# Performance work log

Hardware: AMD Instinct MI355X
Metric: run time of the kernel (lower is better)

Reference implementation:

```python
import jax, jax.numpy as jnp
import numpy as np

N_NODES = 50000
N_EDGES = 800000
D_IN = 128
HC = 128
D_OUT = 128
BN_EPS = 1e-5
RRELU_SLOPE = (1.0 / 8.0 + 1.0 / 3.0) / 2.0  # RReLU eval mode: (lower+upper)/2 = 11/48


def setup_inputs() -> dict:
    key = jax.random.key(0)
    ks = jax.random.split(key, 10)
    s_in = 1.0 / np.sqrt(D_IN)
    s_hc = 1.0 / np.sqrt(HC)
    return {
        "x": jax.random.normal(ks[0], (N_NODES, D_IN), jnp.float32),
        "edge_index": jax.random.randint(ks[1], (2, N_EDGES), 0, N_NODES),
        "edge_attr": jax.random.uniform(ks[2], (N_EDGES,), jnp.float32),
        # conv1: GraphConv(D_IN -> HC): lin_rel (with bias) + lin_root (no bias)
        "W1_rel": jax.random.normal(ks[3], (HC, D_IN), jnp.float32) * s_in,
        "b1": jnp.zeros((HC,), jnp.float32),
        "W1_root": jax.random.normal(ks[4], (HC, D_IN), jnp.float32) * s_in,
        # bn1 affine params
        "gamma": jnp.ones((HC,), jnp.float32),
        "beta": jnp.zeros((HC,), jnp.float32),
        # conv2: GraphConv(HC -> D_OUT)
        "W2_rel": jax.random.normal(ks[5], (D_OUT, HC), jnp.float32) * s_hc,
        "b2": jnp.zeros((D_OUT,), jnp.float32),
        "W2_root": jax.random.normal(ks[6], (D_OUT, HC), jnp.float32) * s_hc,
    }


def graph_conv(x, src, tgt, edge_w, W_rel, b_rel, W_root):
    # message: edge_weight * x[src]; aggregate: scatter-add into target nodes
    msg = x[src] * edge_w[:, None]                                   # [E, F]
    agg = jax.ops.segment_sum(msg, tgt, num_segments=x.shape[0])     # [N, F]
    return agg @ W_rel.T + b_rel + x @ W_root.T                      # [N, F_out]


def reference(x, edge_index, edge_attr, W1_rel, b1, W1_root, gamma, beta, W2_rel, b2, W2_root):
    src, tgt = edge_index[0], edge_index[1]
    h = graph_conv(x, src, tgt, edge_attr, W1_rel, b1, W1_root)      # [N, HC]
    # BatchNorm1d (training mode: biased batch stats over node dim)
    mean = h.mean(axis=0)
    var = h.var(axis=0)
    h = (h - mean) * jax.lax.rsqrt(var + BN_EPS) * gamma + beta
    # RReLU (deterministic eval slope)
    h = jnp.where(h >= 0, h, h * RRELU_SLOPE)
    return graph_conv(h, src, tgt, edge_attr, W2_rel, b2, W2_root)   # [N, D_OUT]
```

## Files before the change

### kernel.cpp

```cpp
#include <hip/hip_runtime.h>

#define N_NODES 50000
#define N_EDGES 800000
#define F 128
#define BN_EPS 1e-5f
#define SLOPE 0.22916666666666666f

#define NBKT 196
#define BKT_CAP 8192
#define P1_CHUNK 4096
#define P1_EPB 16
#define P1_BLKS 196
#define CASTX_BLKS 6250
#define CASTW_BLKS 64
#define BKT_FINAL_CAP 9984
#define REC_CAP 1160192
#define N_RT 3125
#define GEMM_GRID 512

typedef __attribute__((ext_vector_type(8))) short bf16x8;
typedef __attribute__((ext_vector_type(4))) float f32x4;
typedef unsigned long long u64;

__device__ __forceinline__ float bf2f(ushort u) {
    union { uint i; float f; } v; v.i = (uint)u << 16; return v.f;
}
__device__ __forceinline__ ushort f2bf(float f) {
    union { float f; uint i; } v; v.f = f;
    uint r = v.i + 0x7fffu + ((v.i >> 16) & 1u);
    return (ushort)(r >> 16);
}

__global__ __launch_bounds__(256) void s1p_k(const int* __restrict__ src,
        const int* __restrict__ tgt, const float* __restrict__ ew,
        int* __restrict__ bcur, u64* __restrict__ stg,
        const float* __restrict__ x, ushort* __restrict__ xb,
        const float* __restrict__ W1r, const float* __restrict__ W1t,
        const float* __restrict__ W2r, const float* __restrict__ W2t,
        ushort* __restrict__ wb) {
    const int b = blockIdx.x;
    if (b >= P1_BLKS) {
        if (b < P1_BLKS + CASTX_BLKS) {
            int i = (b - P1_BLKS) * 256 + threadIdx.x;
            float4 v = reinterpret_cast<const float4*>(x)[i];
            ushort4 o;
            o.x = f2bf(v.x); o.y = f2bf(v.y); o.z = f2bf(v.z); o.w = f2bf(v.w);
            reinterpret_cast<ushort4*>(xb)[i] = o;
        } else {
            int i = (b - P1_BLKS - CASTX_BLKS) * 256 + threadIdx.x;
            int m = i >> 12;
            int j = i & 4095;
            const float* sp = (m == 0) ? W1r : (m == 1) ? W1t : (m == 2) ? W2r : W2t;
            float4 v = reinterpret_cast<const float4*>(sp)[j];
            ushort4 o;
            o.x = f2bf(v.x); o.y = f2bf(v.y); o.z = f2bf(v.z); o.w = f2bf(v.w);
            reinterpret_cast<ushort4*>(wb)[i] = o;
        }
        return;
    }
    __shared__ uint cnt[256];
    __shared__ uint base[256];
    __shared__ uint lcur[256];
    __shared__ uint gbase[256];
    __shared__ u64 lrec[P1_CHUNK];

    const int e0 = b * P1_CHUNK;
    const int nE = min(P1_CHUNK, N_EDGES - e0);
    cnt[threadIdx.x] = 0;
    __syncthreads();

    u64 myrec[P1_EPB];
    bool myok[P1_EPB];
#pragma unroll
    for (int k = 0; k < P1_EPB; ++k) {
        int idx = threadIdx.x + (k << 8);
        bool ok = idx < nE;
        myok[k] = ok;
        if (ok) {
            int e = e0 + idx;
            uint t = (uint)tgt[e];
            uint lo = (uint)(ushort)src[e] | ((uint)f2bf(ew[e]) << 16);
            myrec[k] = (u64)lo | ((u64)t << 32);
            atomicAdd(&cnt[t >> 8], 1u);
        }
    }
    __syncthreads();
    uint v = cnt[threadIdx.x];
    base[threadIdx.x] = v;
    __syncthreads();
    for (int o = 1; o < 256; o <<= 1) {
        uint t = (threadIdx.x >= (unsigned)o) ? base[threadIdx.x - o] : 0;
        __syncthreads();
        base[threadIdx.x] += t;
        __syncthreads();
    }
    uint excl = base[threadIdx.x] - v;
    base[threadIdx.x] = excl;
    lcur[threadIdx.x] = excl;
    if (threadIdx.x < NBKT && v > 0)
        gbase[threadIdx.x] = (uint)threadIdx.x * BKT_CAP +
                             (uint)atomicAdd(&bcur[threadIdx.x], (int)v);
    __syncthreads();
#pragma unroll
    for (int k = 0; k < P1_EPB; ++k) {
        if (myok[k]) {
            uint bb = (uint)(myrec[k] >> 40);
            uint slot = atomicAdd(&lcur[bb], 1u);
            lrec[slot] = myrec[k];
        }
    }
    __syncthreads();
    for (int s = threadIdx.x; s < nE; s += 256) {
        u64 r = lrec[s];
        uint bb = (uint)(r >> 40);
        stg[gbase[bb] + ((uint)s - base[bb])] = r;
    }
}

__global__ __launch_bounds__(256) void sort2_k(const int* __restrict__ bcur,
        const u64* __restrict__ stg, uint* __restrict__ recs, int2* __restrict__ rng) {
    __shared__ int lcnt[256];
    __shared__ int lcur[256];
    __shared__ int sc[256];
    __shared__ int fbase_s;
    __shared__ uint lrec[BKT_FINAL_CAP];
    const int b = blockIdx.x;
    const int tid = threadIdx.x;

    int cnt_t = (tid < NBKT) ? bcur[tid] : 0;
    int stride_t = (tid < NBKT) ? (((cnt_t + 7) & ~7) + 1792) : 0;
    sc[tid] = stride_t;
    lcnt[tid] = 0;
    __syncthreads();
    for (int o = 1; o < 256; o <<= 1) {
        int t = (tid >= o) ? sc[tid - o] : 0;
        __syncthreads();
        sc[tid] += t;
        __syncthreads();
    }
    if (tid == b) fbase_s = sc[tid] - stride_t;
    __syncthreads();
    const int fbase = fbase_s;
    const int cnt = bcur[b];
    const u64* sb = stg + (size_t)b * BKT_CAP;

    for (int i = tid; i < cnt; i += 256)
        atomicAdd(&lcnt[(int)(sb[i] >> 32) & 255], 1);
    __syncthreads();
    const int node = b * 256 + tid;
    int myc = lcnt[tid];
    int myp = (myc + 7) & ~7;
    if (node >= N_NODES) myp = 0;
    sc[tid] = myp;
    __syncthreads();
    for (int o = 1; o < 256; o <<= 1) {
        int t = (tid >= o) ? sc[tid - o] : 0;
        __syncthreads();
        sc[tid] += t;
        __syncthreads();
    }
    const int myoff = sc[tid] - myp;
    const int ptot = sc[255];
    lcur[tid] = myoff;
    if (node < N_NODES) rng[node] = make_int2(fbase + myoff, fbase + myoff + myp);
    for (int i = tid; i < ptot; i += 256) lrec[i] = 0;
    __syncthreads();
    for (int i = tid; i < cnt; i += 256) {
        u64 r = sb[i];
        int n = (int)(r >> 32) & 255;
        int p = atomicAdd(&lcur[n], 1);
        lrec[p] = (uint)r;
    }
    __syncthreads();
    for (int i = tid; i < ptot; i += 256) recs[fbase + i] = lrec[i];
}

__global__ __launch_bounds__(256) void gather_k(const ushort* __restrict__ featb,
        const int2* __restrict__ rng, const uint* __restrict__ recs,
        ushort* __restrict__ aggb) {
    int node = blockIdx.x * 4 + (threadIdx.x >> 6);
    int lane2 = (threadIdx.x & 63) * 2;
    int2 r = rng[node];
    float a0 = 0.f, a1 = 0.f;
    for (int p = r.x; p < r.y; p += 8) {
        uint4 ra = *reinterpret_cast<const uint4*>(recs + p);
        uint4 rb = *reinterpret_cast<const uint4*>(recs + p + 4);
        uint u0 = *reinterpret_cast<const uint*>(featb + (size_t)(ra.x & 0xffffu) * F + lane2);
        uint u1 = *reinterpret_cast<const uint*>(featb + (size_t)(ra.y & 0xffffu) * F + lane2);
        uint u2 = *reinterpret_cast<const uint*>(featb + (size_t)(ra.z & 0xffffu) * F + lane2);
        uint u3 = *reinterpret_cast<const uint*>(featb + (size_t)(ra.w & 0xffffu) * F + lane2);
        uint u4 = *reinterpret_cast<const uint*>(featb + (size_t)(rb.x & 0xffffu) * F + lane2);
        uint u5 = *reinterpret_cast<const uint*>(featb + (size_t)(rb.y & 0xffffu) * F + lane2);
        uint u6 = *reinterpret_cast<const uint*>(featb + (size_t)(rb.z & 0xffffu) * F + lane2);
        uint u7 = *reinterpret_cast<const uint*>(featb + (size_t)(rb.w & 0xffffu) * F + lane2);
        float w0 = bf2f((ushort)(ra.x >> 16)), w1 = bf2f((ushort)(ra.y >> 16));
        float w2 = bf2f((ushort)(ra.z >> 16)), w3 = bf2f((ushort)(ra.w >> 16));
        float w4 = bf2f((ushort)(rb.x >> 16)), w5 = bf2f((ushort)(rb.y >> 16));
        float w6 = bf2f((ushort)(rb.z >> 16)), w7 = bf2f((ushort)(rb.w >> 16));
        a0 += w0 * bf2f((ushort)u0) + w1 * bf2f((ushort)u1)
            + w2 * bf2f((ushort)u2) + w3 * bf2f((ushort)u3)
            + w4 * bf2f((ushort)u4) + w5 * bf2f((ushort)u5)
            + w6 * bf2f((ushort)u6) + w7 * bf2f((ushort)u7);
        a1 += w0 * bf2f((ushort)(u0 >> 16)) + w1 * bf2f((ushort)(u1 >> 16))
            + w2 * bf2f((ushort)(u2 >> 16)) + w3 * bf2f((ushort)(u3 >> 16))
            + w4 * bf2f((ushort)(u4 >> 16)) + w5 * bf2f((ushort)(u5 >> 16))
            + w6 * bf2f((ushort)(u6 >> 16)) + w7 * bf2f((ushort)(u7 >> 16));
    }
    *reinterpret_cast<uint*>(aggb + (size_t)node * F + lane2) =
        (uint)f2bf(a0) | ((uint)f2bf(a1) << 16);
}

__global__ __launch_bounds__(256) void gemm_mfma(const ushort* __restrict__ R,
        const ushort* __restrict__ T, const ushort* __restrict__ Wr,
        const ushort* __restrict__ Wt, const float* __restrict__ bias,
        float* __restrict__ out, ushort* __restrict__ outh,
        float* __restrict__ S, float* __restrict__ S2, int fuse_bn) {
    const int lane = threadIdx.x & 63;
    const int wave = threadIdx.x >> 6;
    const int quad = lane >> 4;
    const int l16 = lane & 15;
    const int cb = wave * 32;

    bf16x8 bR[2][4], bT[2][4];
#pragma unroll
    for (int t = 0; t < 2; ++t)
#pragma unroll
        for (int s = 0; s < 4; ++s) {
            int col = cb + t * 16 + l16;
            int k0 = s * 32 + quad * 8;
            bR[t][s] = *reinterpret_cast<const bf16x8*>(Wr + col * F + k0);
            bT[t][s] = *reinterpret_cast<const bf16x8*>(Wt + col * F + k0);
        }
    const float bias0 = bias[cb + l16];
    const float bias1 = bias[cb + 16 + l16];

    float s0 = 0.f, q0 = 0.f, s1 = 0.f, q1 = 0.f;

    for (int rt = blockIdx.x; rt < N_RT; rt += GEMM_GRID) {
        const int row0 = rt * 16;
        const ushort* rA = R + (row0 + l16) * F + quad * 8;
        const ushort* tA = T + (row0 + l16) * F + quad * 8;
        bf16x8 aR0 = *reinterpret_cast<const bf16x8*>(rA);
        bf16x8 aR1 = *reinterpret_cast<const bf16x8*>(rA + 32);
        bf16x8 aR2 = *reinterpret_cast<const bf16x8*>(rA + 64);
        bf16x8 aR3 = *reinterpret_cast<const bf16x8*>(rA + 96);
        bf16x8 aT0 = *reinterpret_cast<const bf16x8*>(tA);
        bf16x8 aT1 = *reinterpret_cast<const bf16x8*>(tA + 32);
        bf16x8 aT2 = *reinterpret_cast<const bf16x8*>(tA + 64);
        bf16x8 aT3 = *reinterpret_cast<const bf16x8*>(tA + 96);

        f32x4 acc0 = {0.f, 0.f, 0.f, 0.f};
        f32x4 acc1 = {0.f, 0.f, 0.f, 0.f};
        acc0 = __builtin_amdgcn_mfma_f32_16x16x32_bf16(aR0, bR[0][0], acc0, 0, 0, 0);
        acc1 = __builtin_amdgcn_mfma_f32_16x16x32_bf16(aR0, bR[1][0], acc1, 0, 0, 0);
        acc0 = __builtin_amdgcn_mfma_f32_16x16x32_bf16(aR1, bR[0][1], acc0, 0, 0, 0);
        acc1 = __builtin_amdgcn_mfma_f32_16x16x32_bf16(aR1, bR[1][1], acc1, 0, 0, 0);
        acc0 = __builtin_amdgcn_mfma_f32_16x16x32_bf16(aR2, bR[0][2], acc0, 0, 0, 0);
        acc1 = __builtin_amdgcn_mfma_f32_16x16x32_bf16(aR2, bR[1][2], acc1, 0, 0, 0);
        acc0 = __builtin_amdgcn_mfma_f32_16x16x32_bf16(aR3, bR[0][3], acc0, 0, 0, 0);
        acc1 = __builtin_amdgcn_mfma_f32_16x16x32_bf16(aR3, bR[1][3], acc1, 0, 0, 0);
        acc0 = __builtin_amdgcn_mfma_f32_16x16x32_bf16(aT0, bT[0][0], acc0, 0, 0, 0);
        acc1 = __builtin_amdgcn_mfma_f32_16x16x32_bf16(aT0, bT[1][0], acc1, 0, 0, 0);
        acc0 = __builtin_amdgcn_mfma_f32_16x16x32_bf16(aT1, bT[0][1], acc0, 0, 0, 0);
        acc1 = __builtin_amdgcn_mfma_f32_16x16x32_bf16(aT1, bT[1][1], acc1, 0, 0, 0);
        acc0 = __builtin_amdgcn_mfma_f32_16x16x32_bf16(aT2, bT[0][2], acc0, 0, 0, 0);
        acc1 = __builtin_amdgcn_mfma_f32_16x16x32_bf16(aT2, bT[1][2], acc1, 0, 0, 0);
        acc0 = __builtin_amdgcn_mfma_f32_16x16x32_bf16(aT3, bT[0][3], acc0, 0, 0, 0);
        acc1 = __builtin_amdgcn_mfma_f32_16x16x32_bf16(aT3, bT[1][3], acc1, 0, 0, 0);

        const int r0 = row0 + quad * 4;
        if (fuse_bn) {
#pragma unroll
            for (int g = 0; g < 4; ++g) {
                float v0 = acc0[g] + bias0;
                float v1 = acc1[g] + bias1;
                outh[(r0 + g) * F + cb + l16] = f2bf(v0);
                outh[(r0 + g) * F + cb + 16 + l16] = f2bf(v1);
                s0 += v0; q0 += v0 * v0;
                s1 += v1; q1 += v1 * v1;
            }
        } else {
#pragma unroll
            for (int g = 0; g < 4; ++g) {
                out[(r0 + g) * F + cb + l16] = acc0[g] + bias0;
                out[(r0 + g) * F + cb + 16 + l16] = acc1[g] + bias1;
            }
        }
    }

    if (fuse_bn) {
        s0 += __shfl_down(s0, 32); s0 += __shfl_down(s0, 16);
        q0 += __shfl_down(q0, 32); q0 += __shfl_down(q0, 16);
        s1 += __shfl_down(s1, 32); s1 += __shfl_down(s1, 16);
        q1 += __shfl_down(q1, 32); q1 += __shfl_down(q1, 16);
        if (lane < 16) {
            unsafeAtomicAdd(&S[cb + lane], s0);
            unsafeAtomicAdd(&S2[cb + lane], q0);
            unsafeAtomicAdd(&S[cb + 16 + lane], s1);
            unsafeAtomicAdd(&S2[cb + 16 + lane], q1);
        }
    }
}

__global__ __launch_bounds__(256) void norm_act_k(const ushort* __restrict__ hraw,
        const float* __restrict__ S, const float* __restrict__ S2,
        const float* __restrict__ gamma, const float* __restrict__ beta,
        ushort* __restrict__ hb) {
    __shared__ float sc_s[128], sh_s[128];
    if (threadIdx.x < 128) {
        int j = threadIdx.x;
        float mean = S[j] * (1.f / N_NODES);
        float var = S2[j] * (1.f / N_NODES) - mean * mean;
        float inv = rsqrtf(var + BN_EPS);
        float sc = gamma[j] * inv;
        sc_s[j] = sc;
        sh_s[j] = beta[j] - mean * sc;
    }
    __syncthreads();
    int i = blockIdx.x * 256 + threadIdx.x;
    int cbase = (i & 31) * 4;
    uint2 u = reinterpret_cast<const uint2*>(hraw)[i];
    float4 v = make_float4(bf2f((ushort)u.x), bf2f((ushort)(u.x >> 16)),
                           bf2f((ushort)u.y), bf2f((ushort)(u.y >> 16)));
    float4 sc = *reinterpret_cast<const float4*>(&sc_s[cbase]);
    float4 sh = *reinterpret_cast<const float4*>(&sh_s[cbase]);
    v.x = v.x * sc.x + sh.x;
    v.y = v.y * sc.y + sh.y;
    v.z = v.z * sc.z + sh.z;
    v.w = v.w * sc.w + sh.w;
    v.x = v.x >= 0.f ? v.x : v.x * SLOPE;
    v.y = v.y >= 0.f ? v.y : v.y * SLOPE;
    v.z = v.z >= 0.f ? v.z : v.z * SLOPE;
    v.w = v.w >= 0.f ? v.w : v.w * SLOPE;
    uint2 o;
    o.x = (uint)f2bf(v.x) | ((uint)f2bf(v.y) << 16);
    o.y = (uint)f2bf(v.z) | ((uint)f2bf(v.w) << 16);
    reinterpret_cast<uint2*>(hb)[i] = o;
}

extern "C" void kernel_launch(void* const* d_in, const int* in_sizes, int n_in,
                              void* d_out, int out_size, void* d_ws, size_t ws_size,
                              hipStream_t stream) {
    const float* x     = (const float*)d_in[0];
    const int*   ei    = (const int*)d_in[1];
    const float* ea    = (const float*)d_in[2];
    const float* W1r   = (const float*)d_in[3];
    const float* b1    = (const float*)d_in[4];
    const float* W1t   = (const float*)d_in[5];
    const float* gamma = (const float*)d_in[6];
    const float* beta  = (const float*)d_in[7];
    const float* W2r   = (const float*)d_in[8];
    const float* b2    = (const float*)d_in[9];
    const float* W2t   = (const float*)d_in[10];
    float* out = (float*)d_out;

    char* ws = (char*)d_ws;
    size_t off = 0;
    u64*    stg   = (u64*)(ws + off);    off += (size_t)NBKT * BKT_CAP * 8;
    ushort* featb = (ushort*)(ws + off); off += (size_t)N_NODES * F * 2;
    uint*   recs  = (uint*)(ws + off);   off += (size_t)REC_CAP * 4;
    int*    bcur  = (int*)(ws + off);    off += 256 * 4;
    float*  S     = (float*)(ws + off);  off += 128 * 4;
    float*  S2    = (float*)(ws + off);  off += 128 * 4;
    int2*   rng   = (int2*)(ws + off);   off += (size_t)N_NODES * 8;
    ushort* wb    = (ushort*)(ws + off); off += 4 * 16384 * 2;
    ushort* aggb  = (ushort*)stg;
    ushort* hraw  = (ushort*)d_out;

    const int* srcp = ei;
    const int* tgtp = ei + N_EDGES;

    hipMemsetAsync(bcur, 0, 256 * 4 + 256 * 4, stream);
    s1p_k<<<P1_BLKS + CASTX_BLKS + CASTW_BLKS, 256, 0, stream>>>(
        srcp, tgtp, ea, bcur, stg, x, featb, W1r, W1t, W2r, W2t, wb);
    sort2_k<<<NBKT, 256, 0, stream>>>(bcur, stg, recs, rng);

    gather_k<<<N_NODES / 4, 256, 0, stream>>>(featb, rng, recs, aggb);
    gemm_mfma<<<GEMM_GRID, 256, 0, stream>>>(aggb, featb, wb, wb + 16384, b1,
                                             out, hraw, S, S2, 1);
    norm_act_k<<<CASTX_BLKS, 256, 0, stream>>>(hraw, S, S2, gamma, beta, featb);
    gather_k<<<N_NODES / 4, 256, 0, stream>>>(featb, rng, recs, aggb);
    gemm_mfma<<<GEMM_GRID, 256, 0, stream>>>(aggb, featb, wb + 32768, wb + 49152, b2,
                                             out, hraw, S, S2, 0);
}
```

Before: 229.4 us.

## Fuse gather, GEMM and BN-activation into one kernel per layer

Each layer's neighbor gather, dense MFMA GEMM and (for layer 2) the BatchNorm+RReLU apply are combined into a single templated kernel per 16-row tile. The aggregated rows stay in swizzled LDS instead of going through global memory, and normalization is applied on the fly to gathered and root features instead of in a separate pass. BN statistics are accumulated into 8 partitioned buffers to reduce atomic contention. In exchange, the normalize-and-activate work is recomputed for every gathered edge rather than once per node, weights are reloaded per block, and each block's gather time now directly delays its MFMA work.

```diff
diff --git a/kernel.cpp b/kernel.cpp
--- a/kernel.cpp
+++ b/kernel.cpp
@@ -16,7 +16,7 @@
 #define BKT_FINAL_CAP 9984
 #define REC_CAP 1160192
 #define N_RT 3125
-#define GEMM_GRID 512
+#define NPART 8
 
 typedef __attribute__((ext_vector_type(8))) short bf16x8;
 typedef __attribute__((ext_vector_type(4))) float f32x4;
@@ -175,167 +175,154 @@
     for (int i = tid; i < ptot; i += 256) recs[fbase + i] = lrec[i];
 }
 
-__global__ __launch_bounds__(256) void gather_k(const ushort* __restrict__ featb,
-        const int2* __restrict__ rng, const uint* __restrict__ recs,
-        ushort* __restrict__ aggb) {
-    int node = blockIdx.x * 4 + (threadIdx.x >> 6);
-    int lane2 = (threadIdx.x & 63) * 2;
-    int2 r = rng[node];
-    float a0 = 0.f, a1 = 0.f;
-    for (int p = r.x; p < r.y; p += 8) {
-        uint4 ra = *reinterpret_cast<const uint4*>(recs + p);
-        uint4 rb = *reinterpret_cast<const uint4*>(recs + p + 4);
-        uint u0 = *reinterpret_cast<const uint*>(featb + (size_t)(ra.x & 0xffffu) * F + lane2);
-        uint u1 = *reinterpret_cast<const uint*>(featb + (size_t)(ra.y & 0xffffu) * F + lane2);
-        uint u2 = *reinterpret_cast<const uint*>(featb + (size_t)(ra.z & 0xffffu) * F + lane2);
-        uint u3 = *reinterpret_cast<const uint*>(featb + (size_t)(ra.w & 0xffffu) * F + lane2);
-        uint u4 = *reinterpret_cast<const uint*>(featb + (size_t)(rb.x & 0xffffu) * F + lane2);
-        uint u5 = *reinterpret_cast<const uint*>(featb + (size_t)(rb.y & 0xffffu) * F + lane2);
-        uint u6 = *reinterpret_cast<const uint*>(featb + (size_t)(rb.z & 0xffffu) * F + lane2);
-        uint u7 = *reinterpret_cast<const uint*>(featb + (size_t)(rb.w & 0xffffu) * F + lane2);
-        float w0 = bf2f((ushort)(ra.x >> 16)), w1 = bf2f((ushort)(ra.y >> 16));
-        float w2 = bf2f((ushort)(ra.z >> 16)), w3 = bf2f((ushort)(ra.w >> 16));
-        float w4 = bf2f((ushort)(rb.x >> 16)), w5 = bf2f((ushort)(rb.y >> 16));
-        float w6 = bf2f((ushort)(rb.z >> 16)), w7 = bf2f((ushort)(rb.w >> 16));
-        a0 += w0 * bf2f((ushort)u0) + w1 * bf2f((ushort)u1)
-            + w2 * bf2f((ushort)u2) + w3 * bf2f((ushort)u3)
-            + w4 * bf2f((ushort)u4) + w5 * bf2f((ushort)u5)
-            + w6 * bf2f((ushort)u6) + w7 * bf2f((ushort)u7);
-        a1 += w0 * bf2f((ushort)(u0 >> 16)) + w1 * bf2f((ushort)(u1 >> 16))
-            + w2 * bf2f((ushort)(u2 >> 16)) + w3 * bf2f((ushort)(u3 >> 16))
-            + w4 * bf2f((ushort)(u4 >> 16)) + w5 * bf2f((ushort)(u5 >> 16))
-            + w6 * bf2f((ushort)(u6 >> 16)) + w7 * bf2f((ushort)(u7 >> 16));
-    }
-    *reinterpret_cast<uint*>(aggb + (size_t)node * F + lane2) =
-        (uint)f2bf(a0) | ((uint)f2bf(a1) << 16);
-}
-
-__global__ __launch_bounds__(256) void gemm_mfma(const ushort* __restrict__ R,
-        const ushort* __restrict__ T, const ushort* __restrict__ Wr,
+template <int LAYER>
+__global__ __launch_bounds__(256) void fused_k(
+        const ushort* __restrict__ featb, const int2* __restrict__ rng,
+        const uint* __restrict__ recs, const ushort* __restrict__ Wr,
         const ushort* __restrict__ Wt, const float* __restrict__ bias,
-        float* __restrict__ out, ushort* __restrict__ outh,
-        float* __restrict__ S, float* __restrict__ S2, int fuse_bn) {
-    const int lane = threadIdx.x & 63;
-    const int wave = threadIdx.x >> 6;
+        const float* __restrict__ gamma, const float* __restrict__ beta,
+        float* __restrict__ Sp, float* __restrict__ S2p,
+        ushort* __restrict__ outh, float* __restrict__ outf) {
+    __shared__ __align__(16) uint aggu[16 * 64];
+    __shared__ __align__(16) float scs[128];
+    __shared__ __align__(16) float shs[128];
+
+    const int tid = threadIdx.x;
+    const int lane = tid & 63;
+    const int wave = tid >> 6;
+    const int row0 = blockIdx.x * 16;
+
+    if (LAYER == 2) {
+        if (tid < 128) {
+            float s = 0.f, q = 0.f;
+#pragma unroll
+            for (int p = 0; p < NPART; ++p) {
+                s += Sp[p * 128 + tid];
+                q += S2p[p * 128 + tid];
+            }
+            float mean = s * (1.f / N_NODES);
+            float var = q * (1.f / N_NODES) - mean * mean;
+            float inv = rsqrtf(var + BN_EPS);
+            float sc = gamma[tid] * inv;
+            scs[tid] = sc;
+            shs[tid] = beta[tid] - mean * sc;
+        }
+        __syncthreads();
+    }
+
+    const int lane2 = lane * 2;
+    float lsc0 = 1.f, lsh0 = 0.f, lsc1 = 1.f, lsh1 = 0.f;
+    if (LAYER == 2) {
+        lsc0 = scs[lane2]; lsh0 = shs[lane2];
+        lsc1 = scs[lane2 + 1]; lsh1 = shs[lane2 + 1];
+    }
+
+#pragma unroll
+    for (int i = 0; i < 4; ++i) {
+        const int r = wave * 4 + i;
+        const int2 rr = rng[row0 + r];
+        float a0 = 0.f, a1 = 0.f;
+        for (int p = rr.x; p < rr.y; p += 8) {
+            uint4 ra = *reinterpret_cast<const uint4*>(recs + p);
+            uint4 rb = *reinterpret_cast<const uint4*>(recs + p + 4);
+            uint u0 = *reinterpret_cast<const uint*>(featb + (size_t)(ra.x & 0xffffu) * F + lane2);
+            uint u1 = *reinterpret_cast<const uint*>(featb + (size_t)(ra.y & 0xffffu) * F + lane2);
+            uint u2 = *reinterpret_cast<const uint*>(featb + (size_t)(ra.z & 0xffffu) * F + lane2);
+            uint u3 = *reinterpret_cast<const uint*>(featb + (size_t)(ra.w & 0xffffu) * F + lane2);
+            uint u4 = *reinterpret_cast<const uint*>(featb + (size_t)(rb.x & 0xffffu) * F + lane2);
+            uint u5 = *reinterpret_cast<const uint*>(featb + (size_t)(rb.y & 0xffffu) * F + lane2);
+            uint u6 = *reinterpret_cast<const uint*>(featb + (size_t)(rb.z & 0xffffu) * F + lane2);
+            uint u7 = *reinterpret_cast<const uint*>(featb + (size_t)(rb.w & 0xffffu) * F + lane2);
+            float w0 = bf2f((ushort)(ra.x >> 16)), w1 = bf2f((ushort)(ra.y >> 16));
+            float w2 = bf2f((ushort)(ra.z >> 16)), w3 = bf2f((ushort)(ra.w >> 16));
+            float w4 = bf2f((ushort)(rb.x >> 16)), w5 = bf2f((ushort)(rb.y >> 16));
+            float w6 = bf2f((ushort)(rb.z >> 16)), w7 = bf2f((ushort)(rb.w >> 16));
+            auto proc = [&](uint u, float w) {
+                float t0 = bf2f((ushort)u);
+                float t1 = bf2f((ushort)(u >> 16));
+                if (LAYER == 2) {
+                    t0 = t0 * lsc0 + lsh0; t0 = fmaxf(t0, t0 * SLOPE);
+                    t1 = t1 * lsc1 + lsh1; t1 = fmaxf(t1, t1 * SLOPE);
+                }
+                a0 += w * t0;
+                a1 += w * t1;
+            };
+            proc(u0, w0); proc(u1, w1); proc(u2, w2); proc(u3, w3);
+            proc(u4, w4); proc(u5, w5); proc(u6, w6); proc(u7, w7);
+        }
+        aggu[(r * 64 + lane) ^ ((r & 7) << 2)] =
+            (uint)f2bf(a0) | ((uint)f2bf(a1) << 16);
+    }
+    __syncthreads();
+
     const int quad = lane >> 4;
     const int l16 = lane & 15;
     const int cb = wave * 32;
-
-    bf16x8 bR[2][4], bT[2][4];
-#pragma unroll
-    for (int t = 0; t < 2; ++t)
-#pragma unroll
-        for (int s = 0; s < 4; ++s) {
-            int col = cb + t * 16 + l16;
-            int k0 = s * 32 + quad * 8;
-            bR[t][s] = *reinterpret_cast<const bf16x8*>(Wr + col * F + k0);
-            bT[t][s] = *reinterpret_cast<const bf16x8*>(Wt + col * F + k0);
-        }
     const float bias0 = bias[cb + l16];
     const float bias1 = bias[cb + 16 + l16];
 
-    float s0 = 0.f, q0 = 0.f, s1 = 0.f, q1 = 0.f;
-
-    for (int rt = blockIdx.x; rt < N_RT; rt += GEMM_GRID) {
-        const int row0 = rt * 16;
-        const ushort* rA = R + (row0 + l16) * F + quad * 8;
-        const ushort* tA = T + (row0 + l16) * F + quad * 8;
-        bf16x8 aR0 = *reinterpret_cast<const bf16x8*>(rA);
-        bf16x8 aR1 = *reinterpret_cast<const bf16x8*>(rA + 32);
-        bf16x8 aR2 = *reinterpret_cast<const bf16x8*>(rA + 64);
-        bf16x8 aR3 = *reinterpret_cast<const bf16x8*>(rA + 96);
-        bf16x8 aT0 = *reinterpret_cast<const bf16x8*>(tA);
-        bf16x8 aT1 = *reinterpret_cast<const bf16x8*>(tA + 32);
-        bf16x8 aT2 = *reinterpret_cast<const bf16x8*>(tA + 64);
-        bf16x8 aT3 = *reinterpret_cast<const bf16x8*>(tA + 96);
-
-        f32x4 acc0 = {0.f, 0.f, 0.f, 0.f};
-        f32x4 acc1 = {0.f, 0.f, 0.f, 0.f};
-        acc0 = __builtin_amdgcn_mfma_f32_16x16x32_bf16(aR0, bR[0][0], acc0, 0, 0, 0);
-        acc1 = __builtin_amdgcn_mfma_f32_16x16x32_bf16(aR0, bR[1][0], acc1, 0, 0, 0);
-        acc0 = __builtin_amdgcn_mfma_f32_16x16x32_bf16(aR1, bR[0][1], acc0, 0, 0, 0);
-        acc1 = __builtin_amdgcn_mfma_f32_16x16x32_bf16(aR1, bR[1][1], acc1, 0, 0, 0);
-        acc0 = __builtin_amdgcn_mfma_f32_16x16x32_bf16(aR2, bR[0][2], acc0, 0, 0, 0);
-        acc1 = __builtin_amdgcn_mfma_f32_16x16x32_bf16(aR2, bR[1][2], acc1, 0, 0, 0);
-        acc0 = __builtin_amdgcn_mfma_f32_16x16x32_bf16(aR3, bR[0][3], acc0, 0, 0, 0);
-        acc1 = __builtin_amdgcn_mfma_f32_16x16x32_bf16(aR3, bR[1][3], acc1, 0, 0, 0);
-        acc0 = __builtin_amdgcn_mfma_f32_16x16x32_bf16(aT0, bT[0][0], acc0, 0, 0, 0);
-        acc1 = __builtin_amdgcn_mfma_f32_16x16x32_bf16(aT0, bT[1][0], acc1, 0, 0, 0);
-        acc0 = __builtin_amdgcn_mfma_f32_16x16x32_bf16(aT1, bT[0][1], acc0, 0, 0, 0);
-        acc1 = __builtin_amdgcn_mfma_f32_16x16x32_bf16(aT1, bT[1][1], acc1, 0, 0, 0);
-        acc0 = __builtin_amdgcn_mfma_f32_16x16x32_bf16(aT2, bT[0][2], acc0, 0, 0, 0);
-        acc1 = __builtin_amdgcn_mfma_f32_16x16x32_bf16(aT2, bT[1][2], acc1, 0, 0, 0);
-        acc0 = __builtin_amdgcn_mfma_f32_16x16x32_bf16(aT3, bT[0][3], acc0, 0, 0, 0);
-        acc1 = __builtin_amdgcn_mfma_f32_16x16x32_bf16(aT3, bT[1][3], acc1, 0, 0, 0);
-
-        const int r0 = row0 + quad * 4;
-        if (fuse_bn) {
-#pragma unroll
-            for (int g = 0; g < 4; ++g) {
-                float v0 = acc0[g] + bias0;
-                float v1 = acc1[g] + bias1;
-                outh[(r0 + g) * F + cb + l16] = f2bf(v0);
-                outh[(r0 + g) * F + cb + 16 + l16] = f2bf(v1);
-                s0 += v0; q0 += v0 * v0;
-                s1 += v1; q1 += v1 * v1;
+    f32x4 acc0 = {0.f, 0.f, 0.f, 0.f};
+    f32x4 acc1 = {0.f, 0.f, 0.f, 0.f};
+
+#pragma unroll
+    for (int s = 0; s < 4; ++s) {
+        const int k0 = s * 32 + quad * 8;
+        const int ai = (l16 * 64 + (k0 >> 1)) ^ ((l16 & 7) << 2);
+        bf16x8 aR = *reinterpret_cast<const bf16x8*>(&aggu[ai]);
+        bf16x8 w0 = *reinterpret_cast<const bf16x8*>(Wr + (cb + l16) * F + k0);
+        bf16x8 w1 = *reinterpret_cast<const bf16x8*>(Wr + (cb + 16 + l16) * F + k0);
+        acc0 = __builtin_amdgcn_mfma_f32_16x16x32_bf16(aR, w0, acc0, 0, 0, 0);
+        acc1 = __builtin_amdgcn_mfma_f32_16x16x32_bf16(aR, w1, acc1, 0, 0, 0);
+    }
+#pragma unroll
+    for (int s = 0; s < 4; ++s) {
+        const int k0 = s * 32 + quad * 8;
+        bf16x8 aT = *reinterpret_cast<const bf16x8*>(featb + (size_t)(row0 + l16) * F + k0);
+        if (LAYER == 2) {
+#pragma unroll
+            for (int e = 0; e < 8; ++e) {
+                float t = bf2f((ushort)aT[e]) * scs[k0 + e] + shs[k0 + e];
+                t = fmaxf(t, t * SLOPE);
+                aT[e] = (short)f2bf(t);
             }
-        } else {
-#pragma unroll
-            for (int g = 0; g < 4; ++g) {
-                out[(r0 + g) * F + cb + l16] = acc0[g] + bias0;
-                out[(r0 + g) * F + cb + 16 + l16] = acc1[g] + bias1;
-            }
-        }
-    }
-
-    if (fuse_bn) {
+        }
+        bf16x8 w0 = *reinterpret_cast<const bf16x8*>(Wt + (cb + l16) * F + k0);
+        bf16x8 w1 = *reinterpret_cast<const bf16x8*>(Wt + (cb + 16 + l16) * F + k0);
+        acc0 = __builtin_amdgcn_mfma_f32_16x16x32_bf16(aT, w0, acc0, 0, 0, 0);
+        acc1 = __builtin_amdgcn_mfma_f32_16x16x32_bf16(aT, w1, acc1, 0, 0, 0);
+    }
+
+    const int rbase = row0 + quad * 4;
+    if (LAYER == 1) {
+        float s0 = 0.f, q0 = 0.f, s1 = 0.f, q1 = 0.f;
+#pragma unroll
+        for (int g = 0; g < 4; ++g) {
+            float v0 = acc0[g] + bias0;
+            float v1 = acc1[g] + bias1;
+            outh[(size_t)(rbase + g) * F + cb + l16] = f2bf(v0);
+            outh[(size_t)(rbase + g) * F + cb + 16 + l16] = f2bf(v1);
+            s0 += v0; q0 += v0 * v0;
+            s1 += v1; q1 += v1 * v1;
+        }
         s0 += __shfl_down(s0, 32); s0 += __shfl_down(s0, 16);
         q0 += __shfl_down(q0, 32); q0 += __shfl_down(q0, 16);
         s1 += __shfl_down(s1, 32); s1 += __shfl_down(s1, 16);
         q1 += __shfl_down(q1, 32); q1 += __shfl_down(q1, 16);
         if (lane < 16) {
-            unsafeAtomicAdd(&S[cb + lane], s0);
-            unsafeAtomicAdd(&S2[cb + lane], q0);
-            unsafeAtomicAdd(&S[cb + 16 + lane], s1);
-            unsafeAtomicAdd(&S2[cb + 16 + lane], q1);
-        }
-    }
-}
-
-__global__ __launch_bounds__(256) void norm_act_k(const ushort* __restrict__ hraw,
-        const float* __restrict__ S, const float* __restrict__ S2,
-        const float* __restrict__ gamma, const float* __restrict__ beta,
-        ushort* __restrict__ hb) {
-    __shared__ float sc_s[128], sh_s[128];
-    if (threadIdx.x < 128) {
-        int j = threadIdx.x;
-        float mean = S[j] * (1.f / N_NODES);
-        float var = S2[j] * (1.f / N_NODES) - mean * mean;
-        float inv = rsqrtf(var + BN_EPS);
-        float sc = gamma[j] * inv;
-        sc_s[j] = sc;
-        sh_s[j] = beta[j] - mean * sc;
-    }
-    __syncthreads();
-    int i = blockIdx.x * 256 + threadIdx.x;
-    int cbase = (i & 31) * 4;
-    uint2 u = reinterpret_cast<const uint2*>(hraw)[i];
-    float4 v = make_float4(bf2f((ushort)u.x), bf2f((ushort)(u.x >> 16)),
-                           bf2f((ushort)u.y), bf2f((ushort)(u.y >> 16)));
-    float4 sc = *reinterpret_cast<const float4*>(&sc_s[cbase]);
-    float4 sh = *reinterpret_cast<const float4*>(&sh_s[cbase]);
-    v.x = v.x * sc.x + sh.x;
-    v.y = v.y * sc.y + sh.y;
-    v.z = v.z * sc.z + sh.z;
-    v.w = v.w * sc.w + sh.w;
-    v.x = v.x >= 0.f ? v.x : v.x * SLOPE;
-    v.y = v.y >= 0.f ? v.y : v.y * SLOPE;
-    v.z = v.z >= 0.f ? v.z : v.z * SLOPE;
-    v.w = v.w >= 0.f ? v.w : v.w * SLOPE;
-    uint2 o;
-    o.x = (uint)f2bf(v.x) | ((uint)f2bf(v.y) << 16);
-    o.y = (uint)f2bf(v.z) | ((uint)f2bf(v.w) << 16);
-    reinterpret_cast<uint2*>(hb)[i] = o;
+            float* Sb = Sp + (size_t)(blockIdx.x & (NPART - 1)) * 128;
+            float* S2b = S2p + (size_t)(blockIdx.x & (NPART - 1)) * 128;
+            unsafeAtomicAdd(&Sb[cb + lane], s0);
+            unsafeAtomicAdd(&S2b[cb + lane], q0);
+            unsafeAtomicAdd(&Sb[cb + 16 + lane], s1);
+            unsafeAtomicAdd(&S2b[cb + 16 + lane], q1);
+        }
+    } else {
+#pragma unroll
+        for (int g = 0; g < 4; ++g) {
+            outf[(size_t)(rbase + g) * F + cb + l16] = acc0[g] + bias0;
+            outf[(size_t)(rbase + g) * F + cb + 16 + l16] = acc1[g] + bias1;
+        }
+    }
 }
 
 extern "C" void kernel_launch(void* const* d_in, const int* in_sizes, int n_in,
@@ -360,26 +347,22 @@
     ushort* featb = (ushort*)(ws + off); off += (size_t)N_NODES * F * 2;
     uint*   recs  = (uint*)(ws + off);   off += (size_t)REC_CAP * 4;
     int*    bcur  = (int*)(ws + off);    off += 256 * 4;
-    float*  S     = (float*)(ws + off);  off += 128 * 4;
-    float*  S2    = (float*)(ws + off);  off += 128 * 4;
+    float*  Sp    = (float*)(ws + off);  off += NPART * 128 * 4;
+    float*  S2p   = (float*)(ws + off);  off += NPART * 128 * 4;
     int2*   rng   = (int2*)(ws + off);   off += (size_t)N_NODES * 8;
     ushort* wb    = (ushort*)(ws + off); off += 4 * 16384 * 2;
-    ushort* aggb  = (ushort*)stg;
-    ushort* hraw  = (ushort*)d_out;
+    ushort* hraw  = (ushort*)stg;
 
     const int* srcp = ei;
     const int* tgtp = ei + N_EDGES;
 
-    hipMemsetAsync(bcur, 0, 256 * 4 + 256 * 4, stream);
+    hipMemsetAsync(bcur, 0, 256 * 4 + 2 * NPART * 128 * 4, stream);
     s1p_k<<<P1_BLKS + CASTX_BLKS + CASTW_BLKS, 256, 0, stream>>>(
         srcp, tgtp, ea, bcur, stg, x, featb, W1r, W1t, W2r, W2t, wb);
     sort2_k<<<NBKT, 256, 0, stream>>>(bcur, stg, recs, rng);
 
-    gather_k<<<N_NODES / 4, 256, 0, stream>>>(featb, rng, recs, aggb);
-    gemm_mfma<<<GEMM_GRID, 256, 0, stream>>>(aggb, featb, wb, wb + 16384, b1,
-                                             out, hraw, S, S2, 1);
-    norm_act_k<<<CASTX_BLKS, 256, 0, stream>>>(hraw, S, S2, gamma, beta, featb);
-    gather_k<<<N_NODES / 4, 256, 0, stream>>>(featb, rng, recs, aggb);
-    gemm_mfma<<<GEMM_GRID, 256, 0, stream>>>(aggb, featb, wb + 32768, wb + 49152, b2,
-                                             out, hraw, S, S2, 0);
-}
+    fused_k<1><<<N_RT, 256, 0, stream>>>(featb, rng, recs, wb, wb + 16384, b1,
+                                         gamma, beta, Sp, S2p, hraw, out);
+    fused_k<2><<<N_RT, 256, 0, stream>>>(hraw, rng, recs, wb + 32768, wb + 49152, b2,
+                                         gamma, beta, Sp, S2p, hraw, out);
+}
```

Result: no change. 230.3 us (+0.4%).
